# Performance work log

Hardware: AMD Instinct MI355X
Metric: run time of the kernel (lower is better)

## Reference

```python
import jax, jax.numpy as jnp
import numpy as np


def _gcn_conv(x, edge_index, W, b):
    """PyG-style GCNConv: linear, add self-loops, symmetric norm, scatter-add, bias."""
    n = x.shape[0]
    h = x @ W  # [N, F_out]
    loops = jnp.arange(n, dtype=edge_index.dtype)
    row = jnp.concatenate([edge_index[0], loops])  # source
    col = jnp.concatenate([edge_index[1], loops])  # target
    deg = jax.ops.segment_sum(jnp.ones_like(col, dtype=h.dtype), col, num_segments=n)
    dinv = jnp.where(deg > 0, jax.lax.rsqrt(deg), 0.0)
    norm = dinv[row] * dinv[col]  # [E+N]
    msg = h[row] * norm[:, None]  # edge-wise gather + scale
    out = jax.ops.segment_sum(msg, col, num_segments=n)  # scatter-add
    return out + b


def setup_inputs() -> dict:
    key = jax.random.key(0)
    k1, k2, k3, k4 = jax.random.split(key, 4)
    N, E, F_in, F_out = 50000, 800000, 128, 64
    hidden = 2 * F_out
    x = jax.random.normal(k1, (N, F_in), dtype=jnp.float32)
    edge_index = jax.random.randint(k2, (2, E), 0, N, dtype=jnp.int64)
    # Glorot-ish init for weights
    W1 = jax.random.normal(k3, (F_in, hidden), dtype=jnp.float32) / np.sqrt(F_in)
    b1 = jnp.zeros((hidden,), dtype=jnp.float32)
    W2 = jax.random.normal(k4, (hidden, F_out), dtype=jnp.float32) / np.sqrt(hidden)
    b2 = jnp.zeros((F_out,), dtype=jnp.float32)
    return {"x": x, "edge_index": edge_index, "W1": W1, "b1": b1, "W2": W2, "b2": b2}


def reference(x, edge_index, W1, b1, W2, b2):
    h = _gcn_conv(x, edge_index, W1, b1)
    h = jax.nn.relu(h)
    out = _gcn_conv(h, edge_index, W2, b2)
    return out
```

## Files before the change

kernel.cpp:

```cpp
#include <hip/hip_runtime.h>
#include <stdint.h>


typedef _Float16 h2v   __attribute__((ext_vector_type(2)));
typedef _Float16 h4v   __attribute__((ext_vector_type(4)));
typedef _Float16 f16x8 __attribute__((ext_vector_type(8)));
typedef float    f32x4 __attribute__((ext_vector_type(4)));

__global__ void k_prep(const float* __restrict__ W1, const float* __restrict__ W2,
                       _Float16* __restrict__ WT1, h2v* __restrict__ W2P,
                       uint32_t* __restrict__ bcnt,
                       _Float16* __restrict__ h1, _Float16* __restrict__ h2, int n) {
    int i = blockIdx.x * blockDim.x + threadIdx.x;
    if (i < 256) bcnt[i] = 0u;
    if (i < 128) h1[(size_t)n * 128 + i] = (_Float16)0.f;
    if (i < 64)  h2[(size_t)n * 64  + i] = (_Float16)0.f;
    if (i < 128 * 128) {
        int f = i >> 7, k = i & 127;
        WT1[i] = (_Float16)W1[k * 128 + f];
    }
    if (i < 4096) {
        int k2 = i >> 6, f = i & 63;
        h2v pr;
        pr.x = (_Float16)W2[(2 * k2) * 64 + f];
        pr.y = (_Float16)W2[(2 * k2 + 1) * 64 + f];
        W2P[i] = pr;
    }
}

__global__ __launch_bounds__(256)
void k_bhist(const int* __restrict__ col, uint32_t* __restrict__ bcnt, int E) {
    __shared__ uint32_t h[256];
    const int t = threadIdx.x;
    h[t] = 0u; __syncthreads();
    const int base = blockIdx.x * 4096;
#pragma unroll
    for (int k = 0; k < 16; ++k) {
        int i = base + k * 256 + t;
        if (i < E) atomicAdd(&h[__builtin_nontemporal_load(&col[i]) >> 8], 1u);
    }
    __syncthreads();
    if (h[t]) atomicAdd(&bcnt[t], h[t]);
}

__global__ void k_bscan(const uint32_t* __restrict__ bcnt, uint32_t* __restrict__ boff,
                        uint32_t* __restrict__ bfill, int NB) {
    __shared__ uint32_t s[256];
    const int t = threadIdx.x;
    uint32_t v = (t < NB) ? bcnt[t] : 0u;
    s[t] = v; __syncthreads();
    for (int off = 1; off < 256; off <<= 1) {
        uint32_t u = (t >= off) ? s[t - off] : 0u;
        __syncthreads();
        s[t] += u;
        __syncthreads();
    }
    uint32_t ex = s[t] - v;
    if (t < NB) { boff[t] = ex; bfill[t] = ex; }
    if (t == NB - 1) boff[NB] = s[t];
}

__global__ __launch_bounds__(256)
void k_bin(const int* __restrict__ row, const int* __restrict__ col,
           uint32_t* __restrict__ bfill, uint32_t* __restrict__ ebuf, int E) {
    __shared__ uint32_t hcnt[256], hbase[256];
    const int t = threadIdx.x;
    hcnt[t] = 0u; __syncthreads();
    const int base = blockIdx.x * 4096;
#pragma unroll
    for (int k = 0; k < 16; ++k) {
        int i = base + k * 256 + t;
        if (i < E) atomicAdd(&hcnt[__builtin_nontemporal_load(&col[i]) >> 8], 1u);
    }
    __syncthreads();
    hbase[t] = atomicAdd(&bfill[t], hcnt[t]);
    hcnt[t] = 0u;
    __syncthreads();
#pragma unroll
    for (int k = 0; k < 16; ++k) {
        int i = base + k * 256 + t;
        if (i < E) {
            int c = __builtin_nontemporal_load(&col[i]);
            int r = __builtin_nontemporal_load(&row[i]);
            int b = c >> 8;
            uint32_t slot = hbase[b] + atomicAdd(&hcnt[b], 1u);
            ebuf[slot] = (uint32_t)r | ((uint32_t)(c & 255) << 16);
        }
    }
}

__global__ __launch_bounds__(256)
void k_bucket(const uint32_t* __restrict__ boff, const uint32_t* __restrict__ ebuf,
              uint32_t* __restrict__ rps, uint32_t* __restrict__ rpe,
              float* __restrict__ dinv, uint16_t* __restrict__ esrc, int n) {
    __shared__ uint32_t lcnt[256], lscan[256], lbase[256], lfill[256];
    __shared__ uint32_t s_total;
    const int t = threadIdx.x;
    const int b = blockIdx.x;
    const int base_c = b << 8;
    const int nc = min(256, n - base_c);
    const uint32_t start = boff[b], end = boff[b + 1];
    const uint32_t pstart = (start + (uint32_t)b * 2048u + 7u) & ~7u;

    lcnt[t] = 0u; __syncthreads();
    for (uint32_t i = start + t; i < end; i += 256)
        atomicAdd(&lcnt[ebuf[i] >> 16], 1u);
    __syncthreads();

    const uint32_t v  = lcnt[t];
    const uint32_t pc = (v + 7u) & ~7u;
    lscan[t] = pc; __syncthreads();
    for (int off = 1; off < 256; off <<= 1) {
        uint32_t u = (t >= off) ? lscan[t - off] : 0u;
        __syncthreads();
        lscan[t] += u;
        __syncthreads();
    }
    const uint32_t pex = lscan[t] - pc;
    if (t == 255) s_total = lscan[255];
    if (t < nc) {
        rps[base_c + t]  = pstart + pex;
        rpe[base_c + t]  = pstart + pex + pc;
        dinv[base_c + t] = rsqrtf((float)(v + 1u));
    }
    lbase[t] = pstart + pex;
    lfill[t] = 0u;
    __syncthreads();
    const uint32_t total = s_total;
    for (uint32_t i = t; i < total; i += 256)
        esrc[pstart + i] = (uint16_t)n;
    __syncthreads();
    for (uint32_t i = start + t; i < end; i += 256) {
        uint32_t vv = ebuf[i];
        uint32_t cl = vv >> 16;
        uint32_t slot = lbase[cl] + atomicAdd(&lfill[cl], 1u);
        esrc[slot] = (uint16_t)(vv & 0xffffu);
    }
}

template <int FOUT, typename XT>
__global__ __launch_bounds__(256)
void k_gemm_mfma(const XT* __restrict__ X, const _Float16* __restrict__ WT,
                 const float* __restrict__ dinv, _Float16* __restrict__ H, int n) {
    constexpr int K  = 128;
    constexpr int KP = K + 8;
    constexpr int NT = FOUT / 16;
    __shared__ _Float16 Wl[FOUT * KP];

    const int tid = threadIdx.x;
    for (int i = tid; i < FOUT * (K / 8); i += 256) {
        int f = i / (K / 8), kc = i % (K / 8);
        *reinterpret_cast<f16x8*>(&Wl[f * KP + kc * 8]) =
            *reinterpret_cast<const f16x8*>(&WT[f * K + kc * 8]);
    }
    __syncthreads();

    const int wid  = tid >> 6;
    const int lane = tid & 63;
    const int col  = lane & 15;
    const int krow = lane >> 4;
    const int node = blockIdx.x * 64 + wid * 16 + col;
    const int nld  = node < n ? node : n - 1;

    f32x4 acc[NT];
#pragma unroll
    for (int t = 0; t < NT; ++t) acc[t] = (f32x4){0.f, 0.f, 0.f, 0.f};

#pragma unroll
    for (int ks = 0; ks < 4; ++ks) {
        const int k0 = ks * 32 + krow * 8;
        f16x8 b;
        if constexpr (sizeof(XT) == 4) {
            float4 x0 = *reinterpret_cast<const float4*>(&X[(size_t)nld * K + k0]);
            float4 x1 = *reinterpret_cast<const float4*>(&X[(size_t)nld * K + k0 + 4]);
            b[0] = (_Float16)x0.x; b[1] = (_Float16)x0.y;
            b[2] = (_Float16)x0.z; b[3] = (_Float16)x0.w;
            b[4] = (_Float16)x1.x; b[5] = (_Float16)x1.y;
            b[6] = (_Float16)x1.z; b[7] = (_Float16)x1.w;
        } else {
            b = *reinterpret_cast<const f16x8*>(&X[(size_t)nld * K + k0]);
        }
#pragma unroll
        for (int t = 0; t < NT; ++t) {
            f16x8 a = *reinterpret_cast<const f16x8*>(&Wl[(t * 16 + col) * KP + k0]);
            acc[t] = __builtin_amdgcn_mfma_f32_16x16x32_f16(a, b, acc[t], 0, 0, 0);
        }
    }

    if (node < n) {
        const float dv = dinv[node];
#pragma unroll
        for (int t = 0; t < NT; ++t) {
            h4v hv;
            hv.x = (_Float16)(acc[t][0] * dv);
            hv.y = (_Float16)(acc[t][1] * dv);
            hv.z = (_Float16)(acc[t][2] * dv);
            hv.w = (_Float16)(acc[t][3] * dv);
            *reinterpret_cast<h4v*>(&H[(size_t)node * FOUT + t * 16 + krow * 4]) = hv;
        }
    }
}

__global__ __launch_bounds__(256)
void k_aggmm(const _Float16* __restrict__ H, const uint32_t* __restrict__ rps,
             const uint32_t* __restrict__ rpe, const uint16_t* __restrict__ es,
             const float* __restrict__ dinv, const float* __restrict__ b1,
             const h2v* __restrict__ W2P, _Float16* __restrict__ h2out, int n) {
    __shared__ h2v   W2l[64 * 64];
    __shared__ float2 g1row[4][64];
    const int tid = threadIdx.x;
    for (int i = tid; i < 1024; i += 256)
        reinterpret_cast<uint4*>(W2l)[i] = reinterpret_cast<const uint4*>(W2P)[i];
    __syncthreads();

    const int wid = tid >> 6, lane = tid & 63;
    const int v = blockIdx.x * 4 + wid;
    if (v >= n) return;
    const int c0 = lane * 2;
    int p = (int)rps[v];
    const int e = (int)rpe[v];

    float ax = 0.f, ay = 0.f;
    for (; p + 16 <= e; p += 16) {
        uint4 wa = *reinterpret_cast<const uint4*>(&es[p]);
        uint4 wb = *reinterpret_cast<const uint4*>(&es[p + 8]);
        uint32_t id[16] = { wa.x & 0xffffu, wa.x >> 16, wa.y & 0xffffu, wa.y >> 16,
                            wa.z & 0xffffu, wa.z >> 16, wa.w & 0xffffu, wa.w >> 16,
                            wb.x & 0xffffu, wb.x >> 16, wb.y & 0xffffu, wb.y >> 16,
                            wb.z & 0xffffu, wb.z >> 16, wb.w & 0xffffu, wb.w >> 16 };
        h2v hh[16];
#pragma unroll
        for (int u = 0; u < 16; ++u)
            hh[u] = *reinterpret_cast<const h2v*>(&H[(size_t)id[u] * 128 + c0]);
#pragma unroll
        for (int u = 0; u < 16; ++u) { ax += (float)hh[u].x; ay += (float)hh[u].y; }
    }
    if (p < e) {
        uint4 wa = *reinterpret_cast<const uint4*>(&es[p]);
        uint32_t id[8] = { wa.x & 0xffffu, wa.x >> 16, wa.y & 0xffffu, wa.y >> 16,
                           wa.z & 0xffffu, wa.z >> 16, wa.w & 0xffffu, wa.w >> 16 };
        h2v hh[8];
#pragma unroll
        for (int u = 0; u < 8; ++u)
            hh[u] = *reinterpret_cast<const h2v*>(&H[(size_t)id[u] * 128 + c0]);
#pragma unroll
        for (int u = 0; u < 8; ++u) { ax += (float)hh[u].x; ay += (float)hh[u].y; }
    }
    h2v sv = *reinterpret_cast<const h2v*>(&H[(size_t)v * 128 + c0]);
    ax += (float)sv.x; ay += (float)sv.y;
    const float dv = dinv[v];
    float gx = fmaxf(fmaf(dv, ax, b1[c0]), 0.f);
    float gy = fmaxf(fmaf(dv, ay, b1[c0 + 1]), 0.f);
    g1row[wid][lane] = make_float2(gx, gy);

    float acc = 0.f;
#pragma unroll 8
    for (int k2 = 0; k2 < 64; ++k2) {
        float2 g = g1row[wid][k2];
        h2v w = W2l[k2 * 64 + lane];
        acc += g.x * (float)w.x + g.y * (float)w.y;
    }
    h2out[(size_t)v * 64 + lane] = (_Float16)(dv * acc);
}

__global__ __launch_bounds__(256)
void k_agg64(const _Float16* __restrict__ H, const uint32_t* __restrict__ rps,
             const uint32_t* __restrict__ rpe, const uint16_t* __restrict__ es,
             const float* __restrict__ dinv, const float* __restrict__ bias,
             float* __restrict__ out, int n) {
    int wave = (blockIdx.x * blockDim.x + threadIdx.x) >> 6;
    int lane = threadIdx.x & 63;
    if (wave >= n) return;
    const int v = wave;
    const int half = lane >> 5;
    const int c0 = (lane & 31) * 2;
    int p = (int)rps[v] + half * 8;
    const int e = (int)rpe[v];

    float ax = 0.f, ay = 0.f;
    for (; p + 8 <= e; p += 16) {
        uint4 wa = *reinterpret_cast<const uint4*>(&es[p]);
        uint32_t id[8] = { wa.x & 0xffffu, wa.x >> 16, wa.y & 0xffffu, wa.y >> 16,
                           wa.z & 0xffffu, wa.z >> 16, wa.w & 0xffffu, wa.w >> 16 };
        h2v hh[8];
#pragma unroll
        for (int u = 0; u < 8; ++u)
            hh[u] = *reinterpret_cast<const h2v*>(&H[(size_t)id[u] * 64 + c0]);
#pragma unroll
        for (int u = 0; u < 8; ++u) { ax += (float)hh[u].x; ay += (float)hh[u].y; }
    }
    ax += __shfl_xor(ax, 32);
    ay += __shfl_xor(ay, 32);
    if (lane < 32) {
        h2v sv = *reinterpret_cast<const h2v*>(&H[(size_t)v * 64 + c0]);
        ax += (float)sv.x; ay += (float)sv.y;
        const float dv = dinv[v];
        ax = fmaf(dv, ax, bias[c0]);
        ay = fmaf(dv, ay, bias[c0 + 1]);
        *reinterpret_cast<float2*>(&out[(size_t)v * 64 + c0]) = make_float2(ax, ay);
    }
}

extern "C" void kernel_launch(void* const* d_in, const int* in_sizes, int n_in,
                              void* d_out, int out_size, void* d_ws, size_t ws_size,
                              hipStream_t stream) {
    const float* x  = (const float*)d_in[0];
    const int*   ei = (const int*)d_in[1];
    const float* W1 = (const float*)d_in[2];
    const float* b1 = (const float*)d_in[3];
    const float* W2 = (const float*)d_in[4];
    const float* b2 = (const float*)d_in[5];
    float* out = (float*)d_out;

    const int hidden = in_sizes[3];
    const int fin    = in_sizes[2] / hidden;
    const int n      = in_sizes[0] / fin;
    const int E      = in_sizes[1] / 2;
    const int* rowi = ei;
    const int* coli = ei + E;
    (void)n_in; (void)out_size; (void)ws_size;

    char* ws = (char*)d_ws;
    size_t off = 0;
    auto alloc = [&](size_t bytes) -> void* {
        off = (off + 255) & ~(size_t)255;
        void* p = ws + off;
        off += bytes;
        return p;
    };
    const int NB = (n + 255) >> 8;
    uint32_t*  bcnt = (uint32_t*) alloc(256 * 4);
    uint32_t*  boff = (uint32_t*) alloc(257 * 4);
    uint32_t*  bfill= (uint32_t*) alloc(256 * 4);
    uint32_t*  rps  = (uint32_t*) alloc((size_t)n * 4);
    uint32_t*  rpe  = (uint32_t*) alloc((size_t)n * 4);
    float*     dinv = (float*)    alloc((size_t)n * 4);
    uint32_t*  ebuf = (uint32_t*) alloc((size_t)E * 4);
    uint16_t*  esrc = (uint16_t*) alloc(((size_t)E + (size_t)NB * 2048 + 4096) * 2);
    _Float16*  h1   = (_Float16*) alloc((size_t)(n + 1) * 128 * 2);
    _Float16*  h2   = (_Float16*) alloc((size_t)(n + 1) * 64 * 2);
    _Float16*  WT1  = (_Float16*) alloc(128 * 128 * 2);
    h2v*       W2P  = (h2v*)      alloc(64 * 64 * sizeof(h2v));

    const int NW = (E + 4095) >> 12;

    k_prep  <<<64, 256, 0, stream>>>(W1, W2, WT1, W2P, bcnt, h1, h2, n);
    k_bhist <<<NW, 256, 0, stream>>>(coli, bcnt, E);
    k_bscan <<<1, 256, 0, stream>>>(bcnt, boff, bfill, NB);
    k_bin   <<<NW, 256, 0, stream>>>(rowi, coli, bfill, ebuf, E);
    k_bucket<<<NB, 256, 0, stream>>>(boff, ebuf, rps, rpe, dinv, esrc, n);

    const int gb = (n + 63) / 64;
    k_gemm_mfma<128, float><<<gb, 256, 0, stream>>>(x, WT1, dinv, h1, n);
    k_aggmm <<<(n + 3) / 4, 256, 0, stream>>>(h1, rps, rpe, esrc, dinv, b1, W2P, h2, n);
    k_agg64 <<<(n + 3) / 4, 256, 0, stream>>>(h2, rps, rpe, esrc, dinv, b2, out, n);
}
```

Measured before the change: 197.1 us.

## Widen gather loads and split edges across lanes with fdot2 accumulation

Both aggregation kernels now have each lane load 8 bytes (four fp16 features) per neighbour instead of 4. Different lane groups process different edges of the same 8-edge chunk, and partial sums are combined with cross-lane shuffles. Accumulation and the fused W2 matvec use the packed fp16 dot-product builtin (fdot2), and the hidden row is staged in shared memory as fp16 rather than fp32. The aim is fewer, wider memory transactions and fewer conversion instructions, at the cost of extra shuffle reductions and the intermediate hidden values being rounded to fp16.

```diff
diff --git a/kernel.cpp b/kernel.cpp
--- a/kernel.cpp
+++ b/kernel.cpp
@@ -6,6 +6,21 @@
 typedef _Float16 h4v   __attribute__((ext_vector_type(4)));
 typedef _Float16 f16x8 __attribute__((ext_vector_type(8)));
 typedef float    f32x4 __attribute__((ext_vector_type(4)));
+
+#if defined(__has_builtin)
+#if __has_builtin(__builtin_amdgcn_fdot2)
+#define HAVE_FDOT2 1
+#endif
+#endif
+
+__device__ __forceinline__ float fdot2_acc(h2v a, h2v b, float c) {
+#ifdef HAVE_FDOT2
+    return __builtin_amdgcn_fdot2(a, b, c, false);
+#else
+    return c + (float)a.x * (float)b.x + (float)a.y * (float)b.y;
+#endif
+}
+__device__ __forceinline__ h2v as_h2(uint32_t u) { return __builtin_bit_cast(h2v, u); }
 
 __global__ void k_prep(const float* __restrict__ W1, const float* __restrict__ W2,
                        _Float16* __restrict__ WT1, h2v* __restrict__ W2P,
@@ -206,8 +221,8 @@
              const uint32_t* __restrict__ rpe, const uint16_t* __restrict__ es,
              const float* __restrict__ dinv, const float* __restrict__ b1,
              const h2v* __restrict__ W2P, _Float16* __restrict__ h2out, int n) {
-    __shared__ h2v   W2l[64 * 64];
-    __shared__ float2 g1row[4][64];
+    __shared__ h2v      W2l[64 * 64];
+    __shared__ _Float16 g1row[4][128];
     const int tid = threadIdx.x;
     for (int i = tid; i < 1024; i += 256)
         reinterpret_cast<uint4*>(W2l)[i] = reinterpret_cast<const uint4*>(W2P)[i];
@@ -216,49 +231,59 @@
     const int wid = tid >> 6, lane = tid & 63;
     const int v = blockIdx.x * 4 + wid;
     if (v >= n) return;
-    const int c0 = lane * 2;
+    const uint32_t shift = (lane & 32) ? 16u : 0u;
+    const uint32_t loff  = (uint32_t)(lane & 31) * 8u;
+    const char* Hb = (const char*)H;
+    const h2v one0 = {(_Float16)1.f, (_Float16)0.f};
+    const h2v zero1 = {(_Float16)0.f, (_Float16)1.f};
+
     int p = (int)rps[v];
     const int e = (int)rpe[v];
-
-    float ax = 0.f, ay = 0.f;
-    for (; p + 16 <= e; p += 16) {
-        uint4 wa = *reinterpret_cast<const uint4*>(&es[p]);
-        uint4 wb = *reinterpret_cast<const uint4*>(&es[p + 8]);
-        uint32_t id[16] = { wa.x & 0xffffu, wa.x >> 16, wa.y & 0xffffu, wa.y >> 16,
-                            wa.z & 0xffffu, wa.z >> 16, wa.w & 0xffffu, wa.w >> 16,
-                            wb.x & 0xffffu, wb.x >> 16, wb.y & 0xffffu, wb.y >> 16,
-                            wb.z & 0xffffu, wb.z >> 16, wb.w & 0xffffu, wb.w >> 16 };
-        h2v hh[16];
-#pragma unroll
-        for (int u = 0; u < 16; ++u)
-            hh[u] = *reinterpret_cast<const h2v*>(&H[(size_t)id[u] * 128 + c0]);
-#pragma unroll
-        for (int u = 0; u < 16; ++u) { ax += (float)hh[u].x; ay += (float)hh[u].y; }
-    }
-    if (p < e) {
-        uint4 wa = *reinterpret_cast<const uint4*>(&es[p]);
-        uint32_t id[8] = { wa.x & 0xffffu, wa.x >> 16, wa.y & 0xffffu, wa.y >> 16,
-                           wa.z & 0xffffu, wa.z >> 16, wa.w & 0xffffu, wa.w >> 16 };
-        h2v hh[8];
-#pragma unroll
-        for (int u = 0; u < 8; ++u)
-            hh[u] = *reinterpret_cast<const h2v*>(&H[(size_t)id[u] * 128 + c0]);
-#pragma unroll
-        for (int u = 0; u < 8; ++u) { ax += (float)hh[u].x; ay += (float)hh[u].y; }
-    }
-    h2v sv = *reinterpret_cast<const h2v*>(&H[(size_t)v * 128 + c0]);
-    ax += (float)sv.x; ay += (float)sv.y;
+    float a0 = 0.f, a1 = 0.f, a2 = 0.f, a3 = 0.f;
+
+    for (; p + 8 <= e; p += 8) {
+        const uint4 wa = *reinterpret_cast<const uint4*>(&es[p]);
+        uint32_t dw[4] = {wa.x, wa.y, wa.z, wa.w};
+#pragma unroll
+        for (int j = 0; j < 4; ++j) {
+            uint32_t id  = (dw[j] >> shift) & 0xffffu;
+            uint32_t off = (id << 8) + loff;
+            uint2 u = *reinterpret_cast<const uint2*>(Hb + off);
+            h2v lo = as_h2(u.x), hi = as_h2(u.y);
+            a0 = fdot2_acc(lo, one0,  a0);
+            a1 = fdot2_acc(lo, zero1, a1);
+            a2 = fdot2_acc(hi, one0,  a2);
+            a3 = fdot2_acc(hi, zero1, a3);
+        }
+    }
+    a0 += __shfl_xor(a0, 32); a1 += __shfl_xor(a1, 32);
+    a2 += __shfl_xor(a2, 32); a3 += __shfl_xor(a3, 32);
+
+    {
+        uint2 su = *reinterpret_cast<const uint2*>(Hb + ((uint32_t)v << 8) + loff);
+        h2v lo = as_h2(su.x), hi = as_h2(su.y);
+        a0 = fdot2_acc(lo, one0,  a0);
+        a1 = fdot2_acc(lo, zero1, a1);
+        a2 = fdot2_acc(hi, one0,  a2);
+        a3 = fdot2_acc(hi, zero1, a3);
+    }
     const float dv = dinv[v];
-    float gx = fmaxf(fmaf(dv, ax, b1[c0]), 0.f);
-    float gy = fmaxf(fmaf(dv, ay, b1[c0 + 1]), 0.f);
-    g1row[wid][lane] = make_float2(gx, gy);
+    const float4 bv = *reinterpret_cast<const float4*>(&b1[(lane & 31) * 4]);
+    h4v gh;
+    gh.x = (_Float16)fmaxf(fmaf(dv, a0, bv.x), 0.f);
+    gh.y = (_Float16)fmaxf(fmaf(dv, a1, bv.y), 0.f);
+    gh.z = (_Float16)fmaxf(fmaf(dv, a2, bv.z), 0.f);
+    gh.w = (_Float16)fmaxf(fmaf(dv, a3, bv.w), 0.f);
+    *reinterpret_cast<h4v*>(&g1row[wid][(lane & 31) * 4]) = gh;
 
     float acc = 0.f;
-#pragma unroll 8
-    for (int k2 = 0; k2 < 64; ++k2) {
-        float2 g = g1row[wid][k2];
-        h2v w = W2l[k2 * 64 + lane];
-        acc += g.x * (float)w.x + g.y * (float)w.y;
+#pragma unroll
+    for (int kb = 0; kb < 64; kb += 4) {
+        uint4 gu = *reinterpret_cast<const uint4*>(&g1row[wid][kb * 2]);
+        acc = fdot2_acc(W2l[(kb + 0) * 64 + lane], as_h2(gu.x), acc);
+        acc = fdot2_acc(W2l[(kb + 1) * 64 + lane], as_h2(gu.y), acc);
+        acc = fdot2_acc(W2l[(kb + 2) * 64 + lane], as_h2(gu.z), acc);
+        acc = fdot2_acc(W2l[(kb + 3) * 64 + lane], as_h2(gu.w), acc);
     }
     h2out[(size_t)v * 64 + lane] = (_Float16)(dv * acc);
 }
@@ -272,32 +297,54 @@
     int lane = threadIdx.x & 63;
     if (wave >= n) return;
     const int v = wave;
-    const int half = lane >> 5;
-    const int c0 = (lane & 31) * 2;
-    int p = (int)rps[v] + half * 8;
+    const bool seldw   = (lane & 32) != 0;
+    const uint32_t shift = (lane & 16) ? 16u : 0u;
+    const uint32_t loff  = (uint32_t)(lane & 15) * 8u;
+    const char* Hb = (const char*)H;
+    const h2v one0 = {(_Float16)1.f, (_Float16)0.f};
+    const h2v zero1 = {(_Float16)0.f, (_Float16)1.f};
+
+    int p = (int)rps[v];
     const int e = (int)rpe[v];
-
-    float ax = 0.f, ay = 0.f;
-    for (; p + 8 <= e; p += 16) {
-        uint4 wa = *reinterpret_cast<const uint4*>(&es[p]);
-        uint32_t id[8] = { wa.x & 0xffffu, wa.x >> 16, wa.y & 0xffffu, wa.y >> 16,
-                           wa.z & 0xffffu, wa.z >> 16, wa.w & 0xffffu, wa.w >> 16 };
-        h2v hh[8];
-#pragma unroll
-        for (int u = 0; u < 8; ++u)
-            hh[u] = *reinterpret_cast<const h2v*>(&H[(size_t)id[u] * 64 + c0]);
-#pragma unroll
-        for (int u = 0; u < 8; ++u) { ax += (float)hh[u].x; ay += (float)hh[u].y; }
-    }
-    ax += __shfl_xor(ax, 32);
-    ay += __shfl_xor(ay, 32);
-    if (lane < 32) {
-        h2v sv = *reinterpret_cast<const h2v*>(&H[(size_t)v * 64 + c0]);
-        ax += (float)sv.x; ay += (float)sv.y;
+    float a0 = 0.f, a1 = 0.f, a2 = 0.f, a3 = 0.f;
+
+    for (; p + 8 <= e; p += 8) {
+        const uint4 wa = *reinterpret_cast<const uint4*>(&es[p]);
+        uint32_t d0 = seldw ? wa.y : wa.x;
+        uint32_t d1 = seldw ? wa.w : wa.z;
+#pragma unroll
+        for (int j = 0; j < 2; ++j) {
+            uint32_t d = j ? d1 : d0;
+            uint32_t id  = (d >> shift) & 0xffffu;
+            uint32_t off = (id << 7) + loff;
+            uint2 u = *reinterpret_cast<const uint2*>(Hb + off);
+            h2v lo = as_h2(u.x), hi = as_h2(u.y);
+            a0 = fdot2_acc(lo, one0,  a0);
+            a1 = fdot2_acc(lo, zero1, a1);
+            a2 = fdot2_acc(hi, one0,  a2);
+            a3 = fdot2_acc(hi, zero1, a3);
+        }
+    }
+    a0 += __shfl_xor(a0, 16); a1 += __shfl_xor(a1, 16);
+    a2 += __shfl_xor(a2, 16); a3 += __shfl_xor(a3, 16);
+    a0 += __shfl_xor(a0, 32); a1 += __shfl_xor(a1, 32);
+    a2 += __shfl_xor(a2, 32); a3 += __shfl_xor(a3, 32);
+
+    if (lane < 16) {
+        uint2 su = *reinterpret_cast<const uint2*>(Hb + ((uint32_t)v << 7) + loff);
+        h2v lo = as_h2(su.x), hi = as_h2(su.y);
+        a0 = fdot2_acc(lo, one0,  a0);
+        a1 = fdot2_acc(lo, zero1, a1);
+        a2 = fdot2_acc(hi, one0,  a2);
+        a3 = fdot2_acc(hi, zero1, a3);
         const float dv = dinv[v];
-        ax = fmaf(dv, ax, bias[c0]);
-        ay = fmaf(dv, ay, bias[c0 + 1]);
-        *reinterpret_cast<float2*>(&out[(size_t)v * 64 + c0]) = make_float2(ax, ay);
+        const float4 bv = *reinterpret_cast<const float4*>(&bias[lane * 4]);
+        float4 o;
+        o.x = fmaf(dv, a0, bv.x);
+        o.y = fmaf(dv, a1, bv.y);
+        o.z = fmaf(dv, a2, bv.z);
+        o.w = fmaf(dv, a3, bv.w);
+        *reinterpret_cast<float4*>(&out[(size_t)v * 64 + lane * 4]) = o;
     }
 }
 
```

Result: slower. 207.5 us (+5.3%).
